# Kernel tuning notes

Hardware: AMD Instinct MI355X
Metric: run time of the kernel (lower is better)

The kernel has to match this reference:

```python
import jax, jax.numpy as jnp
import numpy as np

B, SEQ, PRED, N, PATCH, STRIDE = 4, 720, 720, 64, 16, 8
DM, EL = 256, 2
PNUM = (PRED + SEQ - PATCH) // STRIDE + 2  # 180
EPS = 1e-5


def _gelu(x):
    return jax.nn.gelu(x, approximate=False)  # torch nn.GELU default (erf)


def _ln(x, w, b):
    mu = x.mean(-1, keepdims=True)
    var = ((x - mu) ** 2).mean(-1, keepdims=True)
    return (x - mu) / jnp.sqrt(var + EPS) * w + b


def _pos_emb(n, d):
    pos = np.arange(n)[:, None].astype(np.float32)
    div = np.exp(np.arange(0, d, 2).astype(np.float32) * (-np.log(10000.0) / d))
    pe = np.zeros((n, d), np.float32)
    pe[:, 0::2] = np.sin(pos * div)
    pe[:, 1::2] = np.cos(pos * div)
    return jnp.asarray(pe)


def _patch_embed(x, emb_w):
    # x: [B, N, L]; ReplicationPad1d((0, STRIDE)) then unfold(patch_len, stride)
    xp = jnp.concatenate([x, jnp.repeat(x[..., -1:], STRIDE, axis=-1)], axis=-1)
    npatch = (xp.shape[-1] - PATCH) // STRIDE + 1
    idx = jnp.arange(npatch)[:, None] * STRIDE + jnp.arange(PATCH)[None, :]
    patches = xp[..., idx]  # [B, N, npatch, PATCH]
    emb = jnp.einsum('bnpl,ld->bnpd', patches, emb_w) + _pos_emb(npatch, DM)
    return emb.reshape(-1, npatch, DM)  # [B*N, npatch, DM]


def _temp_mix(x, w1, b1, w2, b2, nw, nb):
    # Pnum independent Linear(DM,DM)->GELU->Linear(DM,DM), residual + LayerNorm
    h = _gelu(jnp.einsum('bpd,pde->bpe', x, w1) + b1[None])
    o = jnp.einsum('bpd,pde->bpe', h, w2) + b2[None]
    return _ln(o + x, nw, nb)


def _chan_mix(x, w1, b1, w2, b2, nw, nb):
    # DM independent Linear(PNUM,PNUM)->GELU->Linear(PNUM,PNUM), residual + LayerNorm
    h = _gelu(jnp.einsum('bpd,dpq->bqd', x, w1) + b1.T[None])
    o = jnp.einsum('bpd,dpq->bqd', h, w2) + b2.T[None]
    return _ln(o + x, nw, nb)


def _s_correction(x, x_pre):
    xf = jnp.fft.rfft(x, axis=1, norm='ortho')
    pf = jnp.fft.rfft(x_pre, axis=1, norm='ortho')
    xi = jnp.maximum(jnp.fft.irfft(xf * jnp.conj(xf), axis=1), 0.0)
    pi = jnp.maximum(jnp.fft.irfft(pf * jnp.conj(pf), axis=1), 0.0)
    alpha = (xi * pi).sum(1, keepdims=True) / ((pi * pi).sum(1, keepdims=True) + 0.001)
    return jnp.sqrt(alpha)


def _forward(history_data, future_data, revin_w, revin_b, pred_w, pred_b, emb_w,
             ln_w, ln_b, comb_w, comb_b, head_w, head_b,
             tmd_w1, tmd_b1, tmd_w2, tmd_b2, tmd_nw, tmd_nb,
             cmd_w1, cmd_b1, cmd_w2, cmd_b2, cmd_nw, cmd_nb,
             tmu_w1, tmu_b1, tmu_w2, tmu_b2, tmu_nw, tmu_nb,
             cmu_w1, cmu_b1, cmu_w2, cmu_b2, cmu_nw, cmu_nb):
    x0 = history_data[:, :, :, 0]  # [B, SEQ, N]
    mean = x0.mean(1, keepdims=True)
    stdev = jnp.sqrt(x0.var(1, keepdims=True) + EPS)  # unbiased=False
    xn = (x0 - mean) / stdev * revin_w + revin_b  # RevIN norm (affine)
    x = jnp.einsum('bln,lt->bnt', xn, pred_w) + pred_b  # predict_linear on [B,N,SEQ]
    xi = _patch_embed(x, emb_w)  # [B*N, PNUM, DM]
    x_old = _patch_embed(jnp.transpose(x0, (0, 2, 1)), emb_w)  # [B*N, P_old, DM]
    x_all = jnp.zeros(xi.shape + (EL,), xi.dtype)
    for li in range(EL):
        xud = _temp_mix(xi, tmd_w1[li], tmd_b1[li], tmd_w2[li], tmd_b2[li], tmd_nw[li], tmd_nb[li])
        xud = _chan_mix(xud, cmd_w1[li], cmd_b1[li], cmd_w2[li], cmd_b2[li], cmd_nw[li], cmd_nb[li])
        for j in range(li, -1, -1):
            xud = _temp_mix(xud, tmu_w1[j], tmu_b1[j], tmu_w2[j], tmu_b2[j], tmu_nw[j], tmu_nb[j])
            xud = _chan_mix(xud, cmu_w1[j], cmu_b1[j], cmu_w2[j], cmu_b2[j], cmu_nw[j], cmu_nb[j])
        # faithful to original: inner loop shadows `i`, so the write index is always 0
        x_all = x_all.at[:, :, :, 0].set(xud)
    xc = jnp.einsum('bpde,e->bpd', x_all, comb_w) + comb_b  # comb: Linear(EL, 1)
    p_old = x_old.shape[1]
    xc = _s_correction(_ln(x_old, ln_w, ln_b), _ln(xc[:, :p_old, :], ln_w, ln_b)) * xc
    xr = xc.reshape(-1, N, PNUM, DM).transpose(0, 1, 3, 2)  # [B, N, DM, PNUM]
    out = xr.reshape(xr.shape[0], N, DM * PNUM) @ head_w + head_b  # Flatten_Head -> [B, N, PRED]
    out = jnp.transpose(out, (0, 2, 1))  # [B, PRED, N]
    out = (out - revin_b) / (revin_w + EPS * EPS) * stdev + mean  # RevIN denorm
    return out[:, -PRED:, :][..., None]  # [B, PRED, N, 1]


def setup_inputs() -> dict:
    key = jax.random.key(0)
    ks = iter(jax.random.split(key, 64))
    f = lambda shape, s=0.02: s * jax.random.normal(next(ks), shape, jnp.float32)
    inp = dict(
        history_data=jax.random.normal(next(ks), (B, SEQ, N, 1), jnp.float32),
        future_data=jax.random.normal(next(ks), (B, PRED, N, 1), jnp.float32),
        batch_seen=0, epoch=0, train=0,
        revin_w=jnp.ones((N,), jnp.float32), revin_b=jnp.zeros((N,), jnp.float32),
        pred_w=f((SEQ, SEQ + PRED)), pred_b=jnp.zeros((SEQ + PRED,), jnp.float32),
        emb_w=f((PATCH, DM)),
        ln_w=jnp.ones((DM,), jnp.float32), ln_b=jnp.zeros((DM,), jnp.float32),
        comb_w=f((EL,), 0.5), comb_b=jnp.zeros((), jnp.float32),
        head_w=f((DM * PNUM, PRED), 0.005), head_b=jnp.zeros((PRED,), jnp.float32),
    )
    for pre in ('tmd', 'tmu'):
        inp[pre + '_w1'] = f((EL, PNUM, DM, DM)); inp[pre + '_b1'] = jnp.zeros((EL, PNUM, DM), jnp.float32)
        inp[pre + '_w2'] = f((EL, PNUM, DM, DM)); inp[pre + '_b2'] = jnp.zeros((EL, PNUM, DM), jnp.float32)
        inp[pre + '_nw'] = jnp.ones((EL, DM), jnp.float32); inp[pre + '_nb'] = jnp.zeros((EL, DM), jnp.float32)
    for pre in ('cmd', 'cmu'):
        inp[pre + '_w1'] = f((EL, DM, PNUM, PNUM)); inp[pre + '_b1'] = jnp.zeros((EL, DM, PNUM), jnp.float32)
        inp[pre + '_w2'] = f((EL, DM, PNUM, PNUM)); inp[pre + '_b2'] = jnp.zeros((EL, DM, PNUM), jnp.float32)
        inp[pre + '_nw'] = jnp.ones((EL, DM), jnp.float32); inp[pre + '_nb'] = jnp.zeros((EL, DM), jnp.float32)
    return inp


def reference(history_data, future_data, revin_w, revin_b, pred_w, pred_b, emb_w,
              ln_w, ln_b, comb_w, comb_b, head_w, head_b,
              tmd_w1, tmd_b1, tmd_w2, tmd_b2, tmd_nw, tmd_nb,
              cmd_w1, cmd_b1, cmd_w2, cmd_b2, cmd_nw, cmd_nb,
              tmu_w1, tmu_b1, tmu_w2, tmu_b2, tmu_nw, tmu_nb,
              cmu_w1, cmu_b1, cmu_w2, cmu_b2, cmu_nw, cmu_nb,
              batch_seen, epoch, train):
    return _forward(history_data, future_data, revin_w, revin_b, pred_w, pred_b, emb_w,
                    ln_w, ln_b, comb_w, comb_b, head_w, head_b,
                    tmd_w1, tmd_b1, tmd_w2, tmd_b2, tmd_nw, tmd_nb,
                    cmd_w1, cmd_b1, cmd_w2, cmd_b2, cmd_nw, cmd_nb,
                    tmu_w1, tmu_b1, tmu_w2, tmu_b2, tmu_nw, tmu_nb,
                    cmu_w1, cmu_b1, cmu_w2, cmu_b2, cmu_nw, cmu_nb)
```

## Files before the change

kernel.cpp:

```cpp
#include <hip/hip_runtime.h>
#include <cstdint>
#include <cstddef>

namespace {

constexpr int SEQ_ = 720;
constexpr int N_ = 64;
constexpr int T_ = 1440;
constexpr int P_ = 180;
constexpr int PO_ = 90;
constexpr int D_ = 256;
constexpr int PD_ = P_ * D_;
constexpr float EPS_ = 1e-5f;
constexpr int NTILE_ = 39744;

typedef __attribute__((ext_vector_type(8))) short bf16x8;
typedef __attribute__((ext_vector_type(4))) float f32x4;
typedef __attribute__((ext_vector_type(4))) unsigned short u16x4;

__device__ __forceinline__ float gelu_exact(float x) {
  return 0.5f * x * (1.0f + erff(x * 0.70710678118654752f));
}

__device__ __forceinline__ unsigned short f2bf(float x) {
// ... 18 lines not shown
    float v = hist[(size_t)(b * SEQ_ + l) * N_ + n];
    s += v; s2 += v * v;
  }
  __shared__ float rs[4][64], rq[4][64];
  rs[c][n] = s; rq[c][n] = s2;
  __syncthreads();
  if (tid < 64) {
    float S = rs[0][tid] + rs[1][tid] + rs[2][tid] + rs[3][tid];
    float Q = rq[0][tid] + rq[1][tid] + rq[2][tid] + rq[3][tid];
    float mu = S * (1.f / (float)SEQ_);
    float var = Q * (1.f / (float)SEQ_) - mu * mu;
    float sd = sqrtf(var + EPS_);
    int bn = b * 64 + tid;
    meanA[bn] = mu; stdevA[bn] = sd;
    float a = rw[tid] / sd;
    sA[bn] = a;
    sB[bn] = rb[tid] - mu * a;
  }
}

__global__ __launch_bounds__(256) void pred_kernel(
    const float* __restrict__ hist, const float* __restrict__ predw,
    const float* __restrict__ predb, const float* __restrict__ sA,
    const float* __restrict__ sB, float* __restrict__ xbuf) {
  int b = blockIdx.y;
  int t = blockIdx.x * 32 + (threadIdx.x & 31);
  int ng = threadIdx.x >> 5;
  const float* hb = hist + (size_t)b * SEQ_ * N_ + ng * 8;
  float acc[8] = {0.f,0.f,0.f,0.f,0.f,0.f,0.f,0.f};
  float wsum = 0.f;
  #pragma unroll 4
  for (int l = 0; l < SEQ_; l++) {
    float w = predw[(size_t)l * T_ + t];
    float4 h0 = *reinterpret_cast<const float4*>(hb + (size_t)l * N_);
    float4 h1 = *reinterpret_cast<const float4*>(hb + (size_t)l * N_ + 4);
    acc[0] += h0.x * w; acc[1] += h0.y * w; acc[2] += h0.z * w; acc[3] += h0.w * w;
    acc[4] += h1.x * w; acc[5] += h1.y * w; acc[6] += h1.z * w; acc[7] += h1.w * w;
    wsum += w;
  }
  float pb = predb[t];
  #pragma unroll
  for (int q = 0; q < 8; q++) {
    int bn = b * 64 + ng * 8 + q;
    xbuf[(size_t)bn * T_ + t] = sA[bn] * acc[q] + sB[bn] * wsum + pb;
  }
}

__global__ __launch_bounds__(256) void embed_kernel(
    const float* __restrict__ src, const float* __restrict__ embw,
    unsigned short* __restrict__ dst, int mode,
    float* __restrict__ muX, float* __restrict__ rsX) {
  __shared__ float Es[16 * 256];
  __shared__ float Ss[128];
  __shared__ float pS[15][4], pQ[15][4];
  int bn = blockIdx.y;
  int p0 = blockIdx.x * 15;
  int tid = threadIdx.x;
  for (int i = tid; i < 16 * 256; i += 256) Es[i] = embw[i];
  if (tid < 128) {
    int t = p0 * 8 + tid;
    float v;
    if (mode == 0) {
      int tc = t < T_ ? t : (T_ - 1);
      v = src[(size_t)bn * T_ + tc];
    } else {
      int tc = t < SEQ_ ? t : (SEQ_ - 1);
      int b = bn >> 6, n = bn & 63;
      v = src[(size_t)(b * SEQ_ + tc) * N_ + n];
    }
    Ss[tid] = v;
  }
  __syncthreads();
  int np = (mode == 0) ? P_ : PO_;
  float dv = expf(-0.035977892078032f * (float)(tid & ~1));
  int w = tid >> 6, l = tid & 63;
  for (int pi = 0; pi < 15; pi++) {
    int p = p0 + pi;
    float acc = 0.f;
    #pragma unroll
    for (int k = 0; k < 16; k++) acc += Ss[pi * 8 + k] * Es[k * 256 + tid];
    float ang = (float)p * dv;
    float pe = (tid & 1) ? cosf(ang) : sinf(ang);
    float ov = acc + pe;
    dst[((size_t)bn * np + p) * D_ + tid] = f2bf(ov);
    if (mode == 1) {
      float s = ov, q = ov * ov;
      #pragma unroll
      for (int off = 32; off > 0; off >>= 1) { s += __shfl_xor(s, off); q += __shfl_xor(q, off); }
      if (l == 0) { pS[pi][w] = s; pQ[pi][w] = q; }
    }
  }
  if (mode == 1) {
    __syncthreads();
    if (tid < 15) {
      float S = pS[tid][0] + pS[tid][1] + pS[tid][2] + pS[tid][3];
      float Q = pQ[tid][0] + pQ[tid][1] + pQ[tid][2] + pQ[tid][3];
      float mu = S * (1.f / 256.f);
      int idx = bn * 90 + p0 + tid;
      muX[idx] = mu;
      rsX[idx] = rsqrtf(Q * (1.f / 256.f) - mu * mu + EPS_);
    }
  }
}

struct TileInfo {
  const float* Wg; unsigned short* Og;
  int K, Nn, Kp, k0, n0;
};

__device__ __forceinline__ TileInfo decode_tile(
    int bid,
    const float* t0, const float* t1, const float* t2, const float* t3,
    const float* t4, const float* t5,
    const float* c0, const float* c1, const float* c2, const float* c3,
    const float* c4p, const float* c5, const float* hw,
    unsigned short* WtAll, unsigned short* WcAll, unsigned short* WhAll) {
  TileInfo ti;
  int tk, tn;
  if (bid < 17280) {
    int tt = bid / 2880, rem = bid - tt * 2880;
    int g = rem >> 4, tile = rem & 15;
    const float* s = t0;
    if (tt == 1) s = t1; else if (tt == 2) s = t2; else if (tt == 3) s = t3;
    else if (tt == 4) s = t4; else if (tt == 5) s = t5;
    ti.Wg = s + (size_t)g * 65536;
    ti.Og = WtAll + (size_t)tt * 11796480 + (size_t)g * 65536;
    ti.K = 256; ti.Nn = 256; ti.Kp = 256; tk = tile >> 2; tn = tile & 3;
  } else if (bid < 31104) {
    int b2 = bid - 17280;
    int tt = b2 / 2304, rem = b2 - tt * 2304;
    int g = rem / 9, tile = rem - g * 9;
    const float* s = c0;
    if (tt == 1) s = c1; else if (tt == 2) s = c2; else if (tt == 3) s = c3;
    else if (tt == 4) s = c4p; else if (tt == 5) s = c5;
    ti.Wg = s + (size_t)g * 32400;
    ti.Og = WcAll + (size_t)tt * 9437184 + (size_t)g * 36864;
    ti.K = 180; ti.Nn = 180; ti.Kp = 192; tk = tile / 3; tn = tile - (tile / 3) * 3;
  } else {
    int b2 = bid - 31104;
    ti.Wg = hw; ti.Og = WhAll;
    ti.K = 46080; ti.Nn = 720; ti.Kp = 46080; tk = b2 / 12; tn = b2 - (b2 / 12) * 12;
  }
  ti.k0 = tk * 64; ti.n0 = tn * 64;
  return ti;
}

__global__ __launch_bounds__(256) void convT_all_kernel(
    const float* t0, const float* t1, const float* t2, const float* t3,
    const float* t4, const float* t5,
    const float* c0, const float* c1, const float* c2, const float* c3,
    const float* c4p, const float* c5,
    const float* hw,
    unsigned short* WtAll, unsigned short* WcAll, unsigned short* WhAll,
    int tbase, int tcount) {
  __shared__ float Ts[2][64][65];
  int tid = threadIdx.x;
  int kr = tid >> 4, nc = (tid & 15) * 4;
  int G = gridDim.x;
  int tend = tbase + tcount;

  auto do_load = [&](const TileInfo& ti, float4* r) {
    #pragma unroll
    for (int i = 0; i < 4; i++) {
      int k = ti.k0 + kr + i * 16;
      float4 v = make_float4(0.f, 0.f, 0.f, 0.f);
      if (k < ti.K) {
        int n = ti.n0 + nc;
        if (n + 3 < ti.Nn) {
          v = *reinterpret_cast<const float4*>(ti.Wg + (size_t)k * ti.Nn + n);
        } else {
          if (n + 0 < ti.Nn) v.x = ti.Wg[(size_t)k * ti.Nn + n + 0];
          if (n + 1 < ti.Nn) v.y = ti.Wg[(size_t)k * ti.Nn + n + 1];
          if (n + 2 < ti.Nn) v.z = ti.Wg[(size_t)k * ti.Nn + n + 2];
          if (n + 3 < ti.Nn) v.w = ti.Wg[(size_t)k * ti.Nn + n + 3];
        }
      }
      r[i] = v;
    }
  };

  auto do_write = [&](const float4* r, int b) {
    #pragma unroll
    for (int i = 0; i < 4; i++) {
      Ts[b][kr + i * 16][nc + 0] = r[i].x;
      Ts[b][kr + i * 16][nc + 1] = r[i].y;
      Ts[b][kr + i * 16][nc + 2] = r[i].z;
      Ts[b][kr + i * 16][nc + 3] = r[i].w;
    }
  };

  auto do_store = [&](const TileInfo& ti, int b) {
    #pragma unroll
    for (int it = 0; it < 2; it++) {
      int nr = (tid >> 3) + it * 32;
      int kc = (tid & 7) * 8;
      unsigned int tmp[4];
      #pragma unroll
      for (int j = 0; j < 4; j++) {
        unsigned int lo = f2bf(Ts[b][kc + 2 * j][nr]);
        unsigned int hi = f2bf(Ts[b][kc + 2 * j + 1][nr]);
        tmp[j] = lo | (hi << 16);
      }
      uint4 vv; vv.x = tmp[0]; vv.y = tmp[1]; vv.z = tmp[2]; vv.w = tmp[3];
      *reinterpret_cast<uint4*>(ti.Og + (size_t)(ti.n0 + nr) * ti.Kp + ti.k0 + kc) = vv;
    }
  };

#define DECODE(tt) decode_tile((tt), t0,t1,t2,t3,t4,t5, c0,c1,c2,c3,c4p,c5, hw, WtAll, WcAll, WhAll)

  int t = tbase + blockIdx.x;
  if (t >= tend) return;

  float4 rA[4], rB[4];
  TileInfo i0 = DECODE(t);
  do_load(i0, rA);
  bool v1 = (t + G < tend);
  TileInfo i1 = v1 ? DECODE(t + G) : i0;
  if (v1) do_load(i1, rB);
  do_write(rA, 0);
  bool v2 = (t + 2 * G < tend);
  TileInfo i2 = v2 ? DECODE(t + 2 * G) : i0;
  if (v2) do_load(i2, rA);
  __syncthreads();

  while (true) {
    if (v1) do_write(rB, 1);
    {
      bool v3 = (t + 3 * G < tend);
      TileInfo i3 = i2;
      if (v3) { i3 = DECODE(t + 3 * G); do_load(i3, rB); }
      do_store(i0, 0);
      __syncthreads();
      t += G;
      if (!v1) return;
      i0 = i1; i1 = i2; i2 = i3; v1 = v2; v2 = v3;
    }
    if (v1) do_write(rA, 0);
    {
      bool v3 = (t + 3 * G < tend);
      TileInfo i3 = i2;
      if (v3) { i3 = DECODE(t + 3 * G); do_load(i3, rA); }
      do_store(i0, 1);
      __syncthreads();
      t += G;
      if (!v1) return;
      i0 = i1; i1 = i2; i2 = i3; v1 = v2; v2 = v3;
    }
  }
#undef DECODE
}

__global__ __launch_bounds__(256, 3) void temp_mfma_kernel(
    const unsigned short* __restrict__ X, unsigned short* __restrict__ Y,
    const unsigned short* __restrict__ W1t, const float* __restrict__ B1,
    const unsigned short* __restrict__ W2t, const float* __restrict__ B2,
    const float* __restrict__ NW, const float* __restrict__ NB) {
  __shared__ __align__(16) short Xs[64 * 256];
  __shared__ float partS[64][4];
  __shared__ float partQ[64][4];
  int lin = (blockIdx.x & 7) * 90 + (blockIdx.x >> 3);
  int p = lin >> 2;
  int m0 = (lin & 3) << 6;
  int tid = threadIdx.x;
  int w = tid >> 6, l = tid & 63;
  int lr = l & 15, lq = l >> 4;

  const unsigned short* Xblk = X + (size_t)m0 * PD_ + (size_t)p * D_;
  for (int i = tid; i < 64 * 32; i += 256) {
    int r = i >> 5, c8 = (i & 31) << 3;
    uint4 v = *reinterpret_cast<const uint4*>(Xblk + (size_t)r * PD_ + c8);
    *reinterpret_cast<uint4*>(&Xs[r * 256 + (c8 ^ ((r & 7) << 3))]) = v;
  }
  __syncthreads();

  int n0w = w << 6;
  f32x4 zero4 = {0.f, 0.f, 0.f, 0.f};
  f32x4 acc[4][4];
  #pragma unroll
  for (int a = 0; a < 4; a++)
    #pragma unroll
    for (int b = 0; b < 4; b++) acc[a][b] = zero4;

  const unsigned short* W1p = W1t + (size_t)p * 65536;
  {
    bf16x8 bhc[4], bhn[4];
    #pragma unroll
    for (int nf = 0; nf < 4; nf++)
      bhc[nf] = *reinterpret_cast<const bf16x8*>(W1p + (size_t)(n0w + nf * 16 + lr) * 256 + lq * 8);
    for (int ks = 0; ks < 8; ks++) {
      int kb = ks * 32 + lq * 8;
      bf16x8 af[4];
      #pragma unroll
      for (int mf = 0; mf < 4; mf++) {
        int r = mf * 16 + lr;
        af[mf] = *reinterpret_cast<const bf16x8*>(&Xs[r * 256 + (kb ^ ((r & 7) << 3))]);
      }
      if (ks < 7) {
        #pragma unroll
        for (int nf = 0; nf < 4; nf++)
          bhn[nf] = *reinterpret_cast<const bf16x8*>(W1p + (size_t)(n0w + nf * 16 + lr) * 256 + kb + 32);
      }
      #pragma unroll
      for (int mf = 0; mf < 4; mf++)
        #pragma unroll
        for (int nf = 0; nf < 4; nf++)
          acc[mf][nf] = __builtin_amdgcn_mfma_f32_16x16x32_bf16(af[mf], bhc[nf], acc[mf][nf], 0, 0, 0);
      if (ks < 7) {
        #pragma unroll
        for (int nf = 0; nf < 4; nf++) bhc[nf] = bhn[nf];
      }
    }
  }
  __syncthreads();

  #pragma unroll
  for (int nf = 0; nf < 4; nf++) {
    int n = n0w + nf * 16 + lr;
    float bias = B1[p * 256 + n];
    #pragma unroll
    for (int mf = 0; mf < 4; mf++)
      #pragma unroll
      for (int rg = 0; rg < 4; rg++) {
        int r = mf * 16 + lq * 4 + rg;
        Xs[r * 256 + (n ^ ((r & 7) << 3))] =
            (short)f2bf(gelu_exact(acc[mf][nf][rg] + bias));
      }
  }
  __syncthreads();

  #pragma unroll
  for (int a = 0; a < 4; a++)
    #pragma unroll
    for (int b = 0; b < 4; b++) acc[a][b] = zero4;
  const unsigned short* W2p = W2t + (size_t)p * 65536;
  {
    bf16x8 bhc[4], bhn[4];
    #pragma unroll
    for (int nf = 0; nf < 4; nf++)
      bhc[nf] = *reinterpret_cast<const bf16x8*>(W2p + (size_t)(n0w + nf * 16 + lr) * 256 + lq * 8);
    for (int ks = 0; ks < 8; ks++) {
      int kb = ks * 32 + lq * 8;
      bf16x8 af[4];
      #pragma unroll
      for (int mf = 0; mf < 4; mf++) {
        int r = mf * 16 + lr;
        af[mf] = *reinterpret_cast<const bf16x8*>(&Xs[r * 256 + (kb ^ ((r & 7) << 3))]);
      }
      if (ks < 7) {
        #pragma unroll
        for (int nf = 0; nf < 4; nf++)
          bhn[nf] = *reinterpret_cast<const bf16x8*>(W2p + (size_t)(n0w + nf * 16 + lr) * 256 + kb + 32);
      }
      #pragma unroll
      for (int mf = 0; mf < 4; mf++)
        #pragma unroll
        for (int nf = 0; nf < 4; nf++)
          acc[mf][nf] = __builtin_amdgcn_mfma_f32_16x16x32_bf16(af[mf], bhc[nf], acc[mf][nf], 0, 0, 0);
      if (ks < 7) {
        #pragma unroll
        for (int nf = 0; nf < 4; nf++) bhc[nf] = bhn[nf];
      }
    }
  }

  float b2v[4], nwv[4], nbv[4];
  #pragma unroll
  for (int nf = 0; nf < 4; nf++) {
    int n = n0w + nf * 16 + lr;
    b2v[nf] = B2[p * 256 + n];
    nwv[nf] = NW[n];
    nbv[nf] = NB[n];
  }
  #pragma unroll
  for (int nf = 0; nf < 4; nf++) {
    int n = n0w + nf * 16 + lr;
    #pragma unroll
    for (int mf = 0; mf < 4; mf++)
      #pragma unroll
      for (int rg = 0; rg < 4; rg++) {
        int r = mf * 16 + lq * 4 + rg;
        float res = bf2f(Xblk[(size_t)r * PD_ + n]);
        acc[mf][nf][rg] += b2v[nf] + res;
      }
  }
  #pragma unroll
  for (int mf = 0; mf < 4; mf++)
    #pragma unroll
    for (int rg = 0; rg < 4; rg++) {
      float s = acc[mf][0][rg] + acc[mf][1][rg] + acc[mf][2][rg] + acc[mf][3][rg];
      float q = acc[mf][0][rg] * acc[mf][0][rg] + acc[mf][1][rg] * acc[mf][1][rg] +
                acc[mf][2][rg] * acc[mf][2][rg] + acc[mf][3][rg] * acc[mf][3][rg];
      #pragma unroll
      for (int off = 1; off < 16; off <<= 1) {
        s += __shfl_xor(s, off);
        q += __shfl_xor(q, off);
      }
      if (lr == 0) {
        int r = mf * 16 + lq * 4 + rg;
        partS[r][w] = s;
        partQ[r][w] = q;
      }
    }
  __syncthreads();
  #pragma unroll
  for (int mf = 0; mf < 4; mf++)
    #pragma unroll
    for (int rg = 0; rg < 4; rg++) {
      int r = mf * 16 + lq * 4 + rg;
      float S = partS[r][0] + partS[r][1] + partS[r][2] + partS[r][3];
      float Q = partQ[r][0] + partQ[r][1] + partQ[r][2] + partQ[r][3];
      float mu = S * (1.f / 256.f);
      float rstd = rsqrtf(Q * (1.f / 256.f) - mu * mu + EPS_);
      #pragma unroll
      for (int nf = 0; nf < 4; nf++) {
        int n = n0w + nf * 16 + lr;
        Xs[r * 256 + (n ^ ((r & 7) << 3))] =
            (short)f2bf((acc[mf][nf][rg] - mu) * rstd * nwv[nf] + nbv[nf]);
      }
    }
  __syncthreads();
  unsigned short* Yblk = Y + (size_t)m0 * PD_ + (size_t)p * D_;
  for (int i = tid; i < 64 * 32; i += 256) {
    int r = i >> 5, c8 = (i & 31) << 3;
    uint4 v = *reinterpret_cast<uint4*>(&Xs[r * 256 + (c8 ^ ((r & 7) << 3))]);
    *reinterpret_cast<uint4*>(Yblk + (size_t)r * PD_ + c8) = v;
  }
}

__global__ __launch_bounds__(256) void tr_AB_kernel(
    const unsigned short* __restrict__ A, unsigned short* __restrict__ B16) {
  __shared__ unsigned short T[32][184];
  int bn = blockIdx.y;
  int d0 = blockIdx.x * 32;
  int tid = threadIdx.x;
  int ld = tid & 31, pw = tid >> 5;
  for (int p = pw; p < 180; p += 8)
    T[ld][p] = A[((size_t)bn * 180 + p) * 256 + d0 + ld];
  __syncthreads();
  unsigned int* Bu = reinterpret_cast<unsigned int*>(B16);
  for (int i = tid; i < 32 * 96; i += 256) {
    int r = i / 96, jj = i - r * 96;
    int p0 = 2 * jj;
    unsigned int lo = (p0 < 180) ? (unsigned int)T[r][p0] : 0u;
    unsigned int hi = (p0 + 1 < 180) ? (unsigned int)T[r][p0 + 1] : 0u;
    Bu[((size_t)bn * 256 + d0 + r) * 96 + jj] = lo | (hi << 16);
  }
}

__global__ __launch_bounds__(256, 3) void chan_mfma_kernel(
    const unsigned short* __restrict__ Xb, unsigned short* __restrict__ Yb,
    const unsigned short* __restrict__ W1t, const float* __restrict__ B1,
    const unsigned short* __restrict__ W2t, const float* __restrict__ B2) {
  __shared__ __align__(16) short Xs[64 * 200];
  int lin = (blockIdx.x & 7) * 128 + (blockIdx.x >> 3);
  int d = lin >> 2;
  int m0 = (lin & 3) << 6;
  int tid = threadIdx.x;
  int w = tid >> 6, l = tid & 63;
  int lr = l & 15, lq = l >> 4;

  for (int i = tid; i < 64 * 24; i += 256) {
    int r = i / 24, c = i - r * 24;
    uint4 v = *reinterpret_cast<const uint4*>(
        Xb + ((size_t)(m0 + r) * 256 + d) * 192 + c * 8);
    *reinterpret_cast<uint4*>(&Xs[r * 200 + c * 8]) = v;
  }
  __syncthreads();

  int n0w = w * 48;
  f32x4 zero4 = {0.f, 0.f, 0.f, 0.f};
  f32x4 acc[4][3];
  #pragma unroll
  for (int a = 0; a < 4; a++)
    #pragma unroll
    for (int b = 0; b < 3; b++) acc[a][b] = zero4;

  const unsigned short* W1p = W1t + (size_t)d * (192 * 192);
  {
    bf16x8 bhc[3], bhn[3];
    #pragma unroll
    for (int nf = 0; nf < 3; nf++)
      bhc[nf] = *reinterpret_cast<const bf16x8*>(W1p + (size_t)(n0w + nf * 16 + lr) * 192 + lq * 8);
    for (int ks = 0; ks < 6; ks++) {
      int kb = ks * 32 + lq * 8;
      bf16x8 af[4];
      #pragma unroll
      for (int mf = 0; mf < 4; mf++)
        af[mf] = *reinterpret_cast<const bf16x8*>(&Xs[(mf * 16 + lr) * 200 + kb]);
      if (ks < 5) {
        #pragma unroll
        for (int nf = 0; nf < 3; nf++)
          bhn[nf] = *reinterpret_cast<const bf16x8*>(W1p + (size_t)(n0w + nf * 16 + lr) * 192 + kb + 32);
      }
      #pragma unroll
      for (int mf = 0; mf < 4; mf++)
        #pragma unroll
        for (int nf = 0; nf < 3; nf++)
          acc[mf][nf] = __builtin_amdgcn_mfma_f32_16x16x32_bf16(af[mf], bhc[nf], acc[mf][nf], 0, 0, 0);
      if (ks < 5) {
        #pragma unroll
        for (int nf = 0; nf < 3; nf++) bhc[nf] = bhn[nf];
      }
    }
  }
  __syncthreads();

  #pragma unroll
  for (int nf = 0; nf < 3; nf++) {
    int n = n0w + nf * 16 + lr;
    bool valid = n < 180;
    float bias = valid ? B1[d * 180 + n] : 0.f;
    #pragma unroll
    for (int mf = 0; mf < 4; mf++)
      #pragma unroll
      for (int rg = 0; rg < 4; rg++) {
        int r = mf * 16 + lq * 4 + rg;
        float h = valid ? gelu_exact(acc[mf][nf][rg] + bias) : 0.f;
        Xs[r * 200 + n] = (short)f2bf(h);
      }
  }
  __syncthreads();

  #pragma unroll
  for (int a = 0; a < 4; a++)
    #pragma unroll
    for (int b = 0; b < 3; b++) acc[a][b] = zero4;
  const unsigned short* W2p = W2t + (size_t)d * (192 * 192);
  {
    bf16x8 bhc[3], bhn[3];
    #pragma unroll
    for (int nf = 0; nf < 3; nf++)
      bhc[nf] = *reinterpret_cast<const bf16x8*>(W2p + (size_t)(n0w + nf * 16 + lr) * 192 + lq * 8);
    for (int ks = 0; ks < 6; ks++) {
      int kb = ks * 32 + lq * 8;
      bf16x8 af[4];
      #pragma unroll
      for (int mf = 0; mf < 4; mf++)
        af[mf] = *reinterpret_cast<const bf16x8*>(&Xs[(mf * 16 + lr) * 200 + kb]);
      if (ks < 5) {
        #pragma unroll
        for (int nf = 0; nf < 3; nf++)
          bhn[nf] = *reinterpret_cast<const bf16x8*>(W2p + (size_t)(n0w + nf * 16 + lr) * 192 + kb + 32);
      }
      #pragma unroll
      for (int mf = 0; mf < 4; mf++)
        #pragma unroll
        for (int nf = 0; nf < 3; nf++)
          acc[mf][nf] = __builtin_amdgcn_mfma_f32_16x16x32_bf16(af[mf], bhc[nf], acc[mf][nf], 0, 0, 0);
      if (ks < 5) {
        #pragma unroll
        for (int nf = 0; nf < 3; nf++) bhc[nf] = bhn[nf];
      }
    }
  }

  #pragma unroll
  for (int nf = 0; nf < 3; nf++) {
    int n = n0w + nf * 16 + lr;
    if (n < 180) {
      float b2v = B2[d * 180 + n];
      #pragma unroll
      for (int mf = 0; mf < 4; mf++)
        #pragma unroll
        for (int rg = 0; rg < 4; rg++) {
          int r = mf * 16 + lq * 4 + rg;
          float res = bf2f(Xb[((size_t)(m0 + r) * 256 + d) * 192 + n]);
          Yb[((size_t)(m0 + r) * 256 + d) * 180 + n] = f2bf(acc[mf][nf][rg] + b2v + res);
        }
    }
  }
}

__global__ __launch_bounds__(256) void trLN_kernel(
    const unsigned short* __restrict__ Bsrc, unsigned short* __restrict__ A,
    const float* __restrict__ nw, const float* __restrict__ nb,
    const float* __restrict__ cw, const float* __restrict__ cb, int useComb,
    float* __restrict__ muP, float* __restrict__ rsP) {
  __shared__ float Tl[16][260];
  int bn = blockIdx.y;
  int p0 = blockIdx.x * 16;
  int tid = threadIdx.x;
  int j = tid & 15, db = tid >> 4;
  #pragma unroll 4
  for (int it = 0; it < 16; ++it) {
    int dd = it * 16 + db;
    float v = 0.f;
    if (p0 + j < 180)
      v = bf2f(Bsrc[((size_t)(bn * 256) + dd) * 180 + p0 + j]);
    Tl[j][dd] = v;
  }
  __syncthreads();
  int w = tid >> 6, l = tid & 63;
  float scale = 1.f, shift = 0.f;
  if (useComb) { scale = cw[0]; shift = cb[0]; }
  float4 w4 = *reinterpret_cast<const float4*>(nw + l * 4);
  float4 b4 = *reinterpret_cast<const float4*>(nb + l * 4);
  #pragma unroll
  for (int rr = 0; rr < 4; ++rr) {
    int row = w * 4 + rr;
    int p = p0 + row;
    float4 v = *reinterpret_cast<const float4*>(&Tl[row][l * 4]);
    float s = v.x + v.y + v.z + v.w;
    float s2 = v.x*v.x + v.y*v.y + v.z*v.z + v.w*v.w;
    #pragma unroll
    for (int off = 32; off > 0; off >>= 1) { s += __shfl_xor(s, off); s2 += __shfl_xor(s2, off); }
    float mu = s * (1.f/256.f);
    float rstd = rsqrtf(s2 * (1.f/256.f) - mu * mu + EPS_);
    if (p < 180) {
      float o0 = ((v.x - mu) * rstd * w4.x + b4.x) * scale + shift;
      float o1 = ((v.y - mu) * rstd * w4.y + b4.y) * scale + shift;
      float o2 = ((v.z - mu) * rstd * w4.z + b4.z) * scale + shift;
      float o3 = ((v.w - mu) * rstd * w4.w + b4.w) * scale + shift;
      unsigned int w0 = (unsigned int)f2bf(o0) | ((unsigned int)f2bf(o1) << 16);
      unsigned int w1 = (unsigned int)f2bf(o2) | ((unsigned int)f2bf(o3) << 16);
      unsigned int* dst = reinterpret_cast<unsigned int*>(
          A + ((size_t)bn * 180 + p) * 256 + l * 4);
      dst[0] = w0; dst[1] = w1;
      if (useComb && p < 90) {
        float so = o0 + o1 + o2 + o3;
        float qo = o0*o0 + o1*o1 + o2*o2 + o3*o3;
        #pragma unroll
        for (int off = 32; off > 0; off >>= 1) { so += __shfl_xor(so, off); qo += __shfl_xor(qo, off); }
        if (l == 0) {
          float muo = so * (1.f/256.f);
          muP[bn * 90 + p] = muo;
          rsP[bn * 90 + p] = rsqrtf(qo * (1.f/256.f) - muo * muo + EPS_);
        }
      }
    }
  }
}

__global__ __launch_bounds__(128, 1) void autocorr_kernel(
    const unsigned short* __restrict__ xoldB, const unsigned short* __restrict__ xcB,
    const float* __restrict__ muX, const float* __restrict__ rsX,
    const float* __restrict__ muP, const float* __restrict__ rsP,
    const float* __restrict__ lnw, const float* __restrict__ lnb,
    float* __restrict__ sqa) {
  __shared__ float PI[46][64];
  __shared__ float RED[2][2][64];
  int bn = blockIdx.x >> 2;
  int tid = threadIdx.x;
  int dl = tid & 63;
  int half = tid >> 6;
  int j0 = half * 23;
  int d = ((blockIdx.x & 3) << 6) + dl;
  float w = lnw[d], bb = lnb[d];
  float v[90], wr[90];

  {
    const unsigned short* col = xcB + (size_t)bn * PD_ + d;
    const float* m = muP + bn * 90;
    const float* rs = rsP + bn * 90;
    #pragma unroll
    for (int p = 0; p < 90; p++)
      v[p] = (bf2f(col[(size_t)p * D_]) - m[p]) * rs[p] * w + bb;
    #pragma unroll
    for (int p = 0; p < 90; p++)
      wr[p] = (half == 0) ? v[p] : v[(p + 23) % 90];
  }
  float den = 0.f;
  #pragma unroll 1
  for (int jt = 0; jt < 24; jt += 4) {
    float c0 = 0.f, c1 = 0.f, c2 = 0.f, c3 = 0.f;
    #pragma unroll
    for (int mm = 0; mm < 90; mm++) {
      float vm = v[mm];
      c0 += vm * wr[mm];
      c1 += vm * ((mm + 1 < 90) ? wr[mm + 1] : wr[mm - 89]);
      c2 += vm * ((mm + 2 < 90) ? wr[mm + 2] : wr[mm - 88]);
      c3 += vm * ((mm + 3 < 90) ? wr[mm + 3] : wr[mm - 87]);
    }
    float cq[4] = {c0, c1, c2, c3};
    #pragma unroll
    for (int q = 0; q < 4; q++) {
      if (jt + q < 23) {
        int lag = j0 + jt + q;
        float piv = fmaxf(cq[q] * 0.10540925533894598f, 0.f);
        PI[lag][dl] = piv;
        float wgt = (lag == 0 || lag == 45) ? 1.f : 2.f;
        den += wgt * piv * piv;
      }
    }
    float t0 = wr[0], t1 = wr[1], t2 = wr[2], t3 = wr[3];
    #pragma unroll
    for (int mm = 0; mm < 86; mm++) wr[mm] = wr[mm + 4];
    wr[86] = t0; wr[87] = t1; wr[88] = t2; wr[89] = t3;
  }

  {
    const unsigned short* col = xoldB + (size_t)bn * (PO_ * D_) + d;
    const float* m = muX + bn * 90;
    const float* rs = rsX + bn * 90;
    #pragma unroll
    for (int p = 0; p < 90; p++)
      v[p] = (bf2f(col[(size_t)p * D_]) - m[p]) * rs[p] * w + bb;
    #pragma unroll
    for (int p = 0; p < 90; p++)
      wr[p] = (half == 0) ? v[p] : v[(p + 23) % 90];
  }
  float num = 0.f;
  #pragma unroll 1
  for (int jt = 0; jt < 24; jt += 4) {
    float c0 = 0.f, c1 = 0.f, c2 = 0.f, c3 = 0.f;
    #pragma unroll
// ... 70 lines not shown
  int m0 = mt << 6, n0 = nt << 6;
  int tid = threadIdx.x;
  int w = tid >> 6, l = tid & 63;
  int lr = l & 15, lq = l >> 4;
  f32x4 zero4 = {0.f, 0.f, 0.f, 0.f};
  f32x4 acc[4][4];
  #pragma unroll
  for (int a = 0; a < 4; a++)
    #pragma unroll
    for (int b = 0; b < 4; b++) acc[a][b] = zero4;

  size_t kbase = (size_t)ks * 2880;
  bf16x8 afc[4], bhc[4], afn[4], bhn[4];
  {
    size_t kb = kbase + (size_t)w * 32 + lq * 8;
    #pragma unroll
    for (int mf = 0; mf < 4; mf++)
      afc[mf] = *reinterpret_cast<const bf16x8*>(A + (size_t)(m0 + mf * 16 + lr) * 46080 + kb);
    #pragma unroll
    for (int nf = 0; nf < 4; nf++)
      bhc[nf] = *reinterpret_cast<const bf16x8*>(Bw + (size_t)(n0 + nf * 16 + lr) * 46080 + kb);
  }
  for (int s = w; s < 90; s += 4) {
    int sn = s + 4;
    if (sn < 90) {
      size_t kb = kbase + (size_t)sn * 32 + lq * 8;
      #pragma unroll
      for (int mf = 0; mf < 4; mf++)
        afn[mf] = *reinterpret_cast<const bf16x8*>(A + (size_t)(m0 + mf * 16 + lr) * 46080 + kb);
      #pragma unroll
      for (int nf = 0; nf < 4; nf++)
        bhn[nf] = *reinterpret_cast<const bf16x8*>(Bw + (size_t)(n0 + nf * 16 + lr) * 46080 + kb);
    }
    #pragma unroll
    for (int mf = 0; mf < 4; mf++)
      #pragma unroll
      for (int nf = 0; nf < 4; nf++)
        acc[mf][nf] = __builtin_amdgcn_mfma_f32_16x16x32_bf16(afc[mf], bhc[nf], acc[mf][nf], 0, 0, 0);
    if (sn < 90) {
      #pragma unroll
      for (int mf = 0; mf < 4; mf++) afc[mf] = afn[mf];
      #pragma unroll
      for (int nf = 0; nf < 4; nf++) bhc[nf] = bhn[nf];
    }
  }
  for (int ww = 0; ww < 4; ww++) {
    if (w == ww) {
      #pragma unroll
      for (int mf = 0; mf < 4; mf++)
        #pragma unroll
        for (int nf = 0; nf < 4; nf++)
          #pragma unroll
          for (int rg = 0; rg < 4; rg++) {
            int r = mf * 16 + lq * 4 + rg, c = nf * 16 + lr;
            if (ww == 0) Rs[r][c] = acc[mf][nf][rg];
            else Rs[r][c] += acc[mf][nf][rg];
          }
    }
    __syncthreads();
  }
  for (int i = tid; i < 64 * 64; i += 256) {
    int r = i >> 6, c = i & 63;
    int n = n0 + c;
    if (n < 720)
      P[((size_t)ks * 256 + m0 + r) * 720 + n] = Rs[r][c];
  }
}

__global__ __launch_bounds__(256) void final_kernel(
    const float* __restrict__ P, const float* __restrict__ hb,
    const float* __restrict__ rw, const float* __restrict__ rb,
    const float* __restrict__ meanA, const float* __restrict__ stdevA,
    float* __restrict__ out) {
  int gid = blockIdx.x * 256 + threadIdx.x;
  int bn = gid / 720, t = gid - bn * 720;
  float s = 0.f;
  #pragma unroll
  for (int ks = 0; ks < 16; ks++) s += P[(size_t)ks * 184320 + gid];
  s += hb[t];
  int b = bn >> 6, n = bn & 63;
  float val = (s - rb[n]) / (rw[n] + 1e-10f) * stdevA[bn] + meanA[bn];
  out[((size_t)(b * 720 + t)) * 64 + n] = val;
}

}

extern "C" void kernel_launch(void* const* d_in, const int* in_sizes, int n_in,
                              void* d_out, int out_size, void* d_ws, size_t ws_size,
                              hipStream_t stream) {
  (void)in_sizes; (void)n_in; (void)out_size; (void)ws_size;
  const float* hist   = (const float*)d_in[0];
  const float* revw   = (const float*)d_in[5];
  const float* revb   = (const float*)d_in[6];
  const float* predw  = (const float*)d_in[7];
  const float* predb  = (const float*)d_in[8];
  const float* embw   = (const float*)d_in[9];
  const float* lnw    = (const float*)d_in[10];
  const float* lnb    = (const float*)d_in[11];
  const float* combw  = (const float*)d_in[12];
  const float* combb  = (const float*)d_in[13];
  const float* headw  = (const float*)d_in[14];
  const float* headb  = (const float*)d_in[15];
  const float* tmd_w1 = (const float*)d_in[16];
  const float* tmd_b1 = (const float*)d_in[17];
  const float* tmd_w2 = (const float*)d_in[18];
  const float* tmd_b2 = (const float*)d_in[19];
  const float* tmd_nw = (const float*)d_in[20];
  const float* tmd_nb = (const float*)d_in[21];
  const float* tmu_w1 = (const float*)d_in[22];
  const float* tmu_b1 = (const float*)d_in[23];
  const float* tmu_w2 = (const float*)d_in[24];
  const float* tmu_b2 = (const float*)d_in[25];
  const float* tmu_nw = (const float*)d_in[26];
  const float* tmu_nb = (const float*)d_in[27];
  const float* cmd_w1 = (const float*)d_in[28];
  const float* cmd_b1 = (const float*)d_in[29];
  const float* cmd_w2 = (const float*)d_in[30];
  const float* cmd_b2 = (const float*)d_in[31];
  const float* cmd_nw = (const float*)d_in[32];
  const float* cmd_nb = (const float*)d_in[33];
  const float* cmu_w1 = (const float*)d_in[34];
  const float* cmu_b1 = (const float*)d_in[35];
  const float* cmu_w2 = (const float*)d_in[36];
  const float* cmu_b2 = (const float*)d_in[37];
  const float* cmu_nw = (const float*)d_in[38];
  const float* cmu_nb = (const float*)d_in[39];

  float* ws = (float*)d_ws;
  float* meanA  = ws;
  float* stdevA = meanA + 256;
  float* sA     = stdevA + 256;
  float* sB     = sA + 256;
  float* muX    = sB + 256;
  float* rsX    = muX + 23040;
  float* muP    = rsX + 23040;
  float* rsP    = muP + 23040;
  float* sqa    = rsP + 23040;
  float* xbuf   = sqa + 65536;
  unsigned short* xoldB = (unsigned short*)(xbuf + 368640);
  unsigned short* A0    = xoldB + 5898240;
  unsigned short* A1    = A0 + 11796480;
  unsigned short* B16   = A1 + 11796480;
  unsigned short* Yb    = B16 + 12582912;
  float* part           = (float*)(Yb + 11796480);
  unsigned short* Xtb   = (unsigned short*)(part + 2949120);
  unsigned short* WtAll = Xtb + 11796480;
  unsigned short* WcAll = WtAll + 70778880;
  unsigned short* WhAll = WcAll + 56623104;

  constexpr int TW = 180 * 256 * 256, TB = 180 * 256;
  constexpr int CW = 256 * 180 * 180, CB = 256 * 180;
  constexpr size_t TSTR = 11796480, CSTR = 9437184;

  convT_all_kernel<<<2048, 256, 0, stream>>>(
      tmd_w1 + TW, tmd_w2 + TW, tmu_w1 + TW, tmu_w2 + TW, tmu_w1, tmu_w2,
      cmd_w1 + CW, cmd_w2 + CW, cmu_w1 + CW, cmu_w2 + CW, cmu_w1, cmu_w2,
      headw, WtAll, WcAll, WhAll, 0, NTILE_);

  revin_stats_kernel<<<4, 256, 0, stream>>>(hist, revw, revb, meanA, stdevA, sA, sB);
  pred_kernel<<<dim3(45, 4), 256, 0, stream>>>(hist, predw, predb, sA, sB, xbuf);
  embed_kernel<<<dim3(12, 256), 256, 0, stream>>>(xbuf, embw, A0, 0, nullptr, nullptr);
  embed_kernel<<<dim3(6, 256), 256, 0, stream>>>(hist, embw, xoldB, 1, muX, rsX);

  const float* tB1[3] = {tmd_b1 + TB, tmu_b1 + TB, tmu_b1};
  const float* tB2[3] = {tmd_b2 + TB, tmu_b2 + TB, tmu_b2};
  const float* tNW[3] = {tmd_nw + 256, tmu_nw + 256, tmu_nw};
  const float* tNB[3] = {tmd_nb + 256, tmu_nb + 256, tmu_nb};
  const float* cB1[3] = {cmd_b1 + CB, cmu_b1 + CB, cmu_b1};
  const float* cB2[3] = {cmd_b2 + CB, cmu_b2 + CB, cmu_b2};
  const float* cNW[3] = {cmd_nw + 256, cmu_nw + 256, cmu_nw};
  const float* cNB[3] = {cmd_nb + 256, cmu_nb + 256, cmu_nb};

  for (int li = 0; li < 3; li++) {
    temp_mfma_kernel<<<720, 256, 0, stream>>>(
        A0, A1, WtAll + (size_t)(2 * li) * TSTR, tB1[li],
        WtAll + (size_t)(2 * li + 1) * TSTR, tB2[li], tNW[li], tNB[li]);
    tr_AB_kernel<<<dim3(8, 256), 256, 0, stream>>>(A1, B16);
    chan_mfma_kernel<<<1024, 256, 0, stream>>>(
        B16, Yb, WcAll + (size_t)(2 * li) * CSTR, cB1[li],
        WcAll + (size_t)(2 * li + 1) * CSTR, cB2[li]);
    trLN_kernel<<<dim3(12, 256), 256, 0, stream>>>(Yb, A0, cNW[li], cNB[li],
                                                   combw, combb, li == 2 ? 1 : 0,
                                                   muP, rsP);
  }

  autocorr_kernel<<<1024, 128, 0, stream>>>(xoldB, A0, muX, rsX, muP, rsP, lnw, lnb, sqa);
  scale_tr_kernel<<<dim3(48, 256), 256, 0, stream>>>(A0, sqa, Xtb);
  head_mfma_kernel<<<768, 256, 0, stream>>>(Xtb, WhAll, part);
  final_kernel<<<720, 256, 0, stream>>>(part, headb, revw, revb, meanA, stdevA, (float*)d_out);
}
```

Before: 1.112 ms.

## Split weight transpose into strided phases and prefetch GEMM weights earlier

The single weight-conversion launch becomes four launches, each handling an interleaved subset of tiles with stride 4, which changes the order tiles are touched in memory. In the temp and chan MFMA kernels, the first weight fragments for GEMM1 are loaded before the activation tile is staged into LDS, and the first GEMM2 fragments are loaded before the GELU writeback barrier, so global latency overlaps other work. Launch bounds rise from 3 to 4 blocks per SM, which raises occupancy but may force register spilling. The strided tile split also adds launch overhead and may hurt coalescing.

```diff
diff --git a/kernel.cpp b/kernel.cpp
--- a/kernel.cpp
+++ b/kernel.cpp
@@ -194,12 +194,11 @@
     const float* c4p, const float* c5,
     const float* hw,
     unsigned short* WtAll, unsigned short* WcAll, unsigned short* WhAll,
-    int tbase, int tcount) {
+    int phase, int step) {
   __shared__ float Ts[2][64][65];
   int tid = threadIdx.x;
   int kr = tid >> 4, nc = (tid & 15) * 4;
-  int G = gridDim.x;
-  int tend = tbase + tcount;
+  int S = gridDim.x * step;
 
   auto do_load = [&](const TileInfo& ti, float4* r) {
     #pragma unroll
@@ -250,41 +249,41 @@
 
 #define DECODE(tt) decode_tile((tt), t0,t1,t2,t3,t4,t5, c0,c1,c2,c3,c4p,c5, hw, WtAll, WcAll, WhAll)
 
-  int t = tbase + blockIdx.x;
-  if (t >= tend) return;
+  int t = phase + blockIdx.x * step;
+  if (t >= NTILE_) return;
 
   float4 rA[4], rB[4];
   TileInfo i0 = DECODE(t);
   do_load(i0, rA);
-  bool v1 = (t + G < tend);
-  TileInfo i1 = v1 ? DECODE(t + G) : i0;
+  bool v1 = (t + S < NTILE_);
+  TileInfo i1 = v1 ? DECODE(t + S) : i0;
   if (v1) do_load(i1, rB);
   do_write(rA, 0);
-  bool v2 = (t + 2 * G < tend);
-  TileInfo i2 = v2 ? DECODE(t + 2 * G) : i0;
+  bool v2 = (t + 2 * S < NTILE_);
+  TileInfo i2 = v2 ? DECODE(t + 2 * S) : i0;
   if (v2) do_load(i2, rA);
   __syncthreads();
 
   while (true) {
     if (v1) do_write(rB, 1);
     {
-      bool v3 = (t + 3 * G < tend);
+      bool v3 = (t + 3 * S < NTILE_);
       TileInfo i3 = i2;
-      if (v3) { i3 = DECODE(t + 3 * G); do_load(i3, rB); }
+      if (v3) { i3 = DECODE(t + 3 * S); do_load(i3, rB); }
       do_store(i0, 0);
       __syncthreads();
-      t += G;
+      t += S;
       if (!v1) return;
       i0 = i1; i1 = i2; i2 = i3; v1 = v2; v2 = v3;
     }
     if (v1) do_write(rA, 0);
     {
-      bool v3 = (t + 3 * G < tend);
+      bool v3 = (t + 3 * S < NTILE_);
       TileInfo i3 = i2;
-      if (v3) { i3 = DECODE(t + 3 * G); do_load(i3, rA); }
+      if (v3) { i3 = DECODE(t + 3 * S); do_load(i3, rA); }
       do_store(i0, 1);
       __syncthreads();
-      t += G;
+      t += S;
       if (!v1) return;
       i0 = i1; i1 = i2; i2 = i3; v1 = v2; v2 = v3;
     }
@@ -292,7 +291,7 @@
 #undef DECODE
 }
 
-__global__ __launch_bounds__(256, 3) void temp_mfma_kernel(
+__global__ __launch_bounds__(256, 4) void temp_mfma_kernel(
     const unsigned short* __restrict__ X, unsigned short* __restrict__ Y,
     const unsigned short* __restrict__ W1t, const float* __restrict__ B1,
     const unsigned short* __restrict__ W2t, const float* __restrict__ B2,
@@ -306,6 +305,15 @@
   int tid = threadIdx.x;
   int w = tid >> 6, l = tid & 63;
   int lr = l & 15, lq = l >> 4;
+  int n0w = w << 6;
+
+  const unsigned short* W1p = W1t + (size_t)p * 65536;
+  const unsigned short* W2p = W2t + (size_t)p * 65536;
+
+  bf16x8 bhc[4], bhn[4];
+  #pragma unroll
+  for (int nf = 0; nf < 4; nf++)
+    bhc[nf] = *reinterpret_cast<const bf16x8*>(W1p + (size_t)(n0w + nf * 16 + lr) * 256 + lq * 8);
 
   const unsigned short* Xblk = X + (size_t)m0 * PD_ + (size_t)p * D_;
   for (int i = tid; i < 64 * 32; i += 256) {
@@ -315,7 +323,6 @@
   }
   __syncthreads();
 
-  int n0w = w << 6;
   f32x4 zero4 = {0.f, 0.f, 0.f, 0.f};
   f32x4 acc[4][4];
   #pragma unroll
@@ -323,36 +330,35 @@
     #pragma unroll
     for (int b = 0; b < 4; b++) acc[a][b] = zero4;
 
-  const unsigned short* W1p = W1t + (size_t)p * 65536;
-  {
-    bf16x8 bhc[4], bhn[4];
-    #pragma unroll
-    for (int nf = 0; nf < 4; nf++)
-      bhc[nf] = *reinterpret_cast<const bf16x8*>(W1p + (size_t)(n0w + nf * 16 + lr) * 256 + lq * 8);
-    for (int ks = 0; ks < 8; ks++) {
-      int kb = ks * 32 + lq * 8;
-      bf16x8 af[4];
-      #pragma unroll
-      for (int mf = 0; mf < 4; mf++) {
-        int r = mf * 16 + lr;
-        af[mf] = *reinterpret_cast<const bf16x8*>(&Xs[r * 256 + (kb ^ ((r & 7) << 3))]);
-      }
-      if (ks < 7) {
-        #pragma unroll
-        for (int nf = 0; nf < 4; nf++)
-          bhn[nf] = *reinterpret_cast<const bf16x8*>(W1p + (size_t)(n0w + nf * 16 + lr) * 256 + kb + 32);
-      }
-      #pragma unroll
-      for (int mf = 0; mf < 4; mf++)
-        #pragma unroll
-        for (int nf = 0; nf < 4; nf++)
-          acc[mf][nf] = __builtin_amdgcn_mfma_f32_16x16x32_bf16(af[mf], bhc[nf], acc[mf][nf], 0, 0, 0);
-      if (ks < 7) {
-        #pragma unroll
-        for (int nf = 0; nf < 4; nf++) bhc[nf] = bhn[nf];
-      }
-    }
-  }
+  for (int ks = 0; ks < 8; ks++) {
+    int kb = ks * 32 + lq * 8;
+    bf16x8 af[4];
+    #pragma unroll
+    for (int mf = 0; mf < 4; mf++) {
+      int r = mf * 16 + lr;
+      af[mf] = *reinterpret_cast<const bf16x8*>(&Xs[r * 256 + (kb ^ ((r & 7) << 3))]);
+    }
+    if (ks < 7) {
+      #pragma unroll
+      for (int nf = 0; nf < 4; nf++)
+        bhn[nf] = *reinterpret_cast<const bf16x8*>(W1p + (size_t)(n0w + nf * 16 + lr) * 256 + kb + 32);
+    }
+    #pragma unroll
+    for (int mf = 0; mf < 4; mf++)
+      #pragma unroll
+      for (int nf = 0; nf < 4; nf++)
+        acc[mf][nf] = __builtin_amdgcn_mfma_f32_16x16x32_bf16(af[mf], bhc[nf], acc[mf][nf], 0, 0, 0);
+    if (ks < 7) {
+      #pragma unroll
+      for (int nf = 0; nf < 4; nf++) bhc[nf] = bhn[nf];
+    }
+  }
+
+  bf16x8 bh2[4];
+  #pragma unroll
+  for (int nf = 0; nf < 4; nf++)
+    bh2[nf] = *reinterpret_cast<const bf16x8*>(W2p + (size_t)(n0w + nf * 16 + lr) * 256 + lq * 8);
+
   __syncthreads();
 
   #pragma unroll
@@ -374,34 +380,27 @@
   for (int a = 0; a < 4; a++)
     #pragma unroll
     for (int b = 0; b < 4; b++) acc[a][b] = zero4;
-  const unsigned short* W2p = W2t + (size_t)p * 65536;
-  {
-    bf16x8 bhc[4], bhn[4];
-    #pragma unroll
-    for (int nf = 0; nf < 4; nf++)
-      bhc[nf] = *reinterpret_cast<const bf16x8*>(W2p + (size_t)(n0w + nf * 16 + lr) * 256 + lq * 8);
-    for (int ks = 0; ks < 8; ks++) {
-      int kb = ks * 32 + lq * 8;
-      bf16x8 af[4];
-      #pragma unroll
-      for (int mf = 0; mf < 4; mf++) {
-        int r = mf * 16 + lr;
-        af[mf] = *reinterpret_cast<const bf16x8*>(&Xs[r * 256 + (kb ^ ((r & 7) << 3))]);
-      }
-      if (ks < 7) {
-        #pragma unroll
-        for (int nf = 0; nf < 4; nf++)
-          bhn[nf] = *reinterpret_cast<const bf16x8*>(W2p + (size_t)(n0w + nf * 16 + lr) * 256 + kb + 32);
-      }
-      #pragma unroll
-      for (int mf = 0; mf < 4; mf++)
-        #pragma unroll
-        for (int nf = 0; nf < 4; nf++)
-          acc[mf][nf] = __builtin_amdgcn_mfma_f32_16x16x32_bf16(af[mf], bhc[nf], acc[mf][nf], 0, 0, 0);
-      if (ks < 7) {
-        #pragma unroll
-        for (int nf = 0; nf < 4; nf++) bhc[nf] = bhn[nf];
-      }
+  for (int ks = 0; ks < 8; ks++) {
+    int kb = ks * 32 + lq * 8;
+    bf16x8 af[4];
+    #pragma unroll
+    for (int mf = 0; mf < 4; mf++) {
+      int r = mf * 16 + lr;
+      af[mf] = *reinterpret_cast<const bf16x8*>(&Xs[r * 256 + (kb ^ ((r & 7) << 3))]);
+    }
+    if (ks < 7) {
+      #pragma unroll
+      for (int nf = 0; nf < 4; nf++)
+        bhn[nf] = *reinterpret_cast<const bf16x8*>(W2p + (size_t)(n0w + nf * 16 + lr) * 256 + kb + 32);
+    }
+    #pragma unroll
+    for (int mf = 0; mf < 4; mf++)
+      #pragma unroll
+      for (int nf = 0; nf < 4; nf++)
+        acc[mf][nf] = __builtin_amdgcn_mfma_f32_16x16x32_bf16(af[mf], bh2[nf], acc[mf][nf], 0, 0, 0);
+    if (ks < 7) {
+      #pragma unroll
+      for (int nf = 0; nf < 4; nf++) bh2[nf] = bhn[nf];
     }
   }
 
@@ -489,7 +488,7 @@
   }
 }
 
-__global__ __launch_bounds__(256, 3) void chan_mfma_kernel(
+__global__ __launch_bounds__(256, 4) void chan_mfma_kernel(
     const unsigned short* __restrict__ Xb, unsigned short* __restrict__ Yb,
     const unsigned short* __restrict__ W1t, const float* __restrict__ B1,
     const unsigned short* __restrict__ W2t, const float* __restrict__ B2) {
@@ -500,6 +499,15 @@
   int tid = threadIdx.x;
   int w = tid >> 6, l = tid & 63;
   int lr = l & 15, lq = l >> 4;
+  int n0w = w * 48;
+
+  const unsigned short* W1p = W1t + (size_t)d * (192 * 192);
+  const unsigned short* W2p = W2t + (size_t)d * (192 * 192);
+
+  bf16x8 bhc[3], bhn[3];
+  #pragma unroll
+  for (int nf = 0; nf < 3; nf++)
+    bhc[nf] = *reinterpret_cast<const bf16x8*>(W1p + (size_t)(n0w + nf * 16 + lr) * 192 + lq * 8);
 
   for (int i = tid; i < 64 * 24; i += 256) {
     int r = i / 24, c = i - r * 24;
@@ -509,7 +517,6 @@
   }
   __syncthreads();
 
-  int n0w = w * 48;
   f32x4 zero4 = {0.f, 0.f, 0.f, 0.f};
   f32x4 acc[4][3];
   #pragma unroll
@@ -517,34 +524,33 @@
     #pragma unroll
     for (int b = 0; b < 3; b++) acc[a][b] = zero4;
 
-  const unsigned short* W1p = W1t + (size_t)d * (192 * 192);
-  {
-    bf16x8 bhc[3], bhn[3];
-    #pragma unroll
-    for (int nf = 0; nf < 3; nf++)
-      bhc[nf] = *reinterpret_cast<const bf16x8*>(W1p + (size_t)(n0w + nf * 16 + lr) * 192 + lq * 8);
-    for (int ks = 0; ks < 6; ks++) {
-      int kb = ks * 32 + lq * 8;
-      bf16x8 af[4];
-      #pragma unroll
-      for (int mf = 0; mf < 4; mf++)
-        af[mf] = *reinterpret_cast<const bf16x8*>(&Xs[(mf * 16 + lr) * 200 + kb]);
-      if (ks < 5) {
-        #pragma unroll
-        for (int nf = 0; nf < 3; nf++)
-          bhn[nf] = *reinterpret_cast<const bf16x8*>(W1p + (size_t)(n0w + nf * 16 + lr) * 192 + kb + 32);
-      }
-      #pragma unroll
-      for (int mf = 0; mf < 4; mf++)
-        #pragma unroll
-        for (int nf = 0; nf < 3; nf++)
-          acc[mf][nf] = __builtin_amdgcn_mfma_f32_16x16x32_bf16(af[mf], bhc[nf], acc[mf][nf], 0, 0, 0);
-      if (ks < 5) {
-        #pragma unroll
-        for (int nf = 0; nf < 3; nf++) bhc[nf] = bhn[nf];
-      }
-    }
-  }
+  for (int ks = 0; ks < 6; ks++) {
+    int kb = ks * 32 + lq * 8;
+    bf16x8 af[4];
+    #pragma unroll
+    for (int mf = 0; mf < 4; mf++)
+      af[mf] = *reinterpret_cast<const bf16x8*>(&Xs[(mf * 16 + lr) * 200 + kb]);
+    if (ks < 5) {
+      #pragma unroll
+      for (int nf = 0; nf < 3; nf++)
+        bhn[nf] = *reinterpret_cast<const bf16x8*>(W1p + (size_t)(n0w + nf * 16 + lr) * 192 + kb + 32);
+    }
+    #pragma unroll
+    for (int mf = 0; mf < 4; mf++)
+      #pragma unroll
+      for (int nf = 0; nf < 3; nf++)
+        acc[mf][nf] = __builtin_amdgcn_mfma_f32_16x16x32_bf16(af[mf], bhc[nf], acc[mf][nf], 0, 0, 0);
+    if (ks < 5) {
+      #pragma unroll
+      for (int nf = 0; nf < 3; nf++) bhc[nf] = bhn[nf];
+    }
+  }
+
+  bf16x8 bh2[3];
+  #pragma unroll
+  for (int nf = 0; nf < 3; nf++)
+    bh2[nf] = *reinterpret_cast<const bf16x8*>(W2p + (size_t)(n0w + nf * 16 + lr) * 192 + lq * 8);
+
   __syncthreads();
 
   #pragma unroll
@@ -567,32 +573,25 @@
   for (int a = 0; a < 4; a++)
     #pragma unroll
     for (int b = 0; b < 3; b++) acc[a][b] = zero4;
-  const unsigned short* W2p = W2t + (size_t)d * (192 * 192);
-  {
-    bf16x8 bhc[3], bhn[3];
-    #pragma unroll
-    for (int nf = 0; nf < 3; nf++)
-      bhc[nf] = *reinterpret_cast<const bf16x8*>(W2p + (size_t)(n0w + nf * 16 + lr) * 192 + lq * 8);
-    for (int ks = 0; ks < 6; ks++) {
-      int kb = ks * 32 + lq * 8;
-      bf16x8 af[4];
-      #pragma unroll
-      for (int mf = 0; mf < 4; mf++)
-        af[mf] = *reinterpret_cast<const bf16x8*>(&Xs[(mf * 16 + lr) * 200 + kb]);
-      if (ks < 5) {
-        #pragma unroll
-        for (int nf = 0; nf < 3; nf++)
-          bhn[nf] = *reinterpret_cast<const bf16x8*>(W2p + (size_t)(n0w + nf * 16 + lr) * 192 + kb + 32);
-      }
-      #pragma unroll
-      for (int mf = 0; mf < 4; mf++)
-        #pragma unroll
-        for (int nf = 0; nf < 3; nf++)
-          acc[mf][nf] = __builtin_amdgcn_mfma_f32_16x16x32_bf16(af[mf], bhc[nf], acc[mf][nf], 0, 0, 0);
-      if (ks < 5) {
-        #pragma unroll
-        for (int nf = 0; nf < 3; nf++) bhc[nf] = bhn[nf];
-      }
+  for (int ks = 0; ks < 6; ks++) {
+    int kb = ks * 32 + lq * 8;
+    bf16x8 af[4];
+    #pragma unroll
+    for (int mf = 0; mf < 4; mf++)
+      af[mf] = *reinterpret_cast<const bf16x8*>(&Xs[(mf * 16 + lr) * 200 + kb]);
+    if (ks < 5) {
+      #pragma unroll
+      for (int nf = 0; nf < 3; nf++)
+        bhn[nf] = *reinterpret_cast<const bf16x8*>(W2p + (size_t)(n0w + nf * 16 + lr) * 192 + kb + 32);
+    }
+    #pragma unroll
+    for (int mf = 0; mf < 4; mf++)
+      #pragma unroll
+      for (int nf = 0; nf < 3; nf++)
+        acc[mf][nf] = __builtin_amdgcn_mfma_f32_16x16x32_bf16(af[mf], bh2[nf], acc[mf][nf], 0, 0, 0);
+    if (ks < 5) {
+      #pragma unroll
+      for (int nf = 0; nf < 3; nf++) bh2[nf] = bhn[nf];
     }
   }
 
@@ -969,10 +968,12 @@
   constexpr int CW = 256 * 180 * 180, CB = 256 * 180;
   constexpr size_t TSTR = 11796480, CSTR = 9437184;
 
-  convT_all_kernel<<<2048, 256, 0, stream>>>(
-      tmd_w1 + TW, tmd_w2 + TW, tmu_w1 + TW, tmu_w2 + TW, tmu_w1, tmu_w2,
-      cmd_w1 + CW, cmd_w2 + CW, cmu_w1 + CW, cmu_w2 + CW, cmu_w1, cmu_w2,
-      headw, WtAll, WcAll, WhAll, 0, NTILE_);
+  for (int ph = 0; ph < 4; ph++) {
+    convT_all_kernel<<<2048, 256, 0, stream>>>(
+        tmd_w1 + TW, tmd_w2 + TW, tmu_w1 + TW, tmu_w2 + TW, tmu_w1, tmu_w2,
+        cmd_w1 + CW, cmd_w2 + CW, cmu_w1 + CW, cmu_w2 + CW, cmu_w1, cmu_w2,
+        headw, WtAll, WcAll, WhAll, ph, 4);
+  }
 
   revin_stats_kernel<<<4, 256, 0, stream>>>(hist, revw, revb, meanA, stdevA, sA, sB);
   pred_kernel<<<dim3(45, 4), 256, 0, stream>>>(hist, predw, predb, sA, sB, xbuf);
```

Measured after the change: 1.228 ms. 1.1x slower.
